# Optimization experiments

Hardware: AMD Instinct MI355X
Metric: run time of the kernel (lower is better)

The kernel has to match this reference:

```python
import jax, jax.numpy as jnp
import numpy as np

NUM_HEADS = 16


def rotate_half(x):
    x1 = x[..., ::2]
    x2 = x[..., 1::2]
    return jnp.concatenate((-x2, x1), axis=-1)


def rope_sin_cos(seq_len, head_dim, dtype):
    inv_freq = 1.0 / (10000.0 ** (jnp.arange(0, head_dim, 2, dtype=jnp.float32) / head_dim))
    t = jnp.arange(seq_len, dtype=jnp.float32)
    freqs = jnp.einsum('i,j->ij', t, inv_freq)          # [S, D/2]
    emb = jnp.concatenate((freqs, freqs), axis=-1)      # [S, D]
    return jnp.sin(emb).astype(dtype), jnp.cos(emb).astype(dtype)


def setup_inputs() -> dict:
    key = jax.random.key(0)
    B, S, E = 2, 2048, 2048
    ks = jax.random.split(key, 5)
    scale = 1.0 / np.sqrt(E)
    return {
        'x': jax.random.normal(ks[0], (B, S, E), dtype=jnp.float32),
        'mask': jnp.ones((B, S), dtype=jnp.int32),
        'Wq': jax.random.normal(ks[1], (E, E), dtype=jnp.float32) * scale,
        'bq': jnp.zeros((E,), dtype=jnp.float32),
        'Wk': jax.random.normal(ks[2], (E, E), dtype=jnp.float32) * scale,
        'bk': jnp.zeros((E,), dtype=jnp.float32),
        'Wv': jax.random.normal(ks[3], (E, E), dtype=jnp.float32) * scale,
        'bv': jnp.zeros((E,), dtype=jnp.float32),
        'Wo': jax.random.normal(ks[4], (E, E), dtype=jnp.float32) * scale,
        'bo': jnp.zeros((E,), dtype=jnp.float32),
    }


def reference(x, mask, Wq, bq, Wk, bk, Wv, bv, Wo, bo):
    B, S, E = x.shape
    H = NUM_HEADS
    D = E // H
    q = (x @ Wq + bq).reshape(B, S, H, D).transpose(0, 2, 1, 3)  # [B,H,S,D]
    k = (x @ Wk + bk).reshape(B, S, H, D).transpose(0, 2, 1, 3)
    v = (x @ Wv + bv).reshape(B, S, H, D).transpose(0, 2, 1, 3)

    sin, cos = rope_sin_cos(S, D, q.dtype)  # [S,D]
    sin = sin[None, None]                    # [1,1,S,D]
    cos = cos[None, None]
    q = q * cos + rotate_half(q) * sin
    k = k * cos + rotate_half(k) * sin

    scores = jnp.einsum('bhqd,bhkd->bhqk', q, k) / jnp.sqrt(jnp.asarray(D, q.dtype))
    scores = jnp.where(mask[:, None, None, :] == 0, -jnp.inf, scores)
    probs = jax.nn.softmax(scores, axis=-1)
    attn = jnp.einsum('bhqk,bhkd->bhqd', probs, v)       # [B,H,S,D]
    attn = attn.transpose(0, 2, 1, 3).reshape(B, S, E)
    return attn @ Wo + bo
```

## Files before the change

### kernel.cpp

```cpp
#include <hip/hip_runtime.h>
#include <hip/hip_bf16.h>
#include <cmath>

typedef unsigned short u16;
typedef unsigned int   u32;

using v4f    = __attribute__((ext_vector_type(4)))  float;
using f32x16 = __attribute__((ext_vector_type(16))) float;
using s8v    = __attribute__((ext_vector_type(8)))  short;
using u32x2  = __attribute__((ext_vector_type(2)))  unsigned int;

union Frag { uint4 u; s8v s; };

__device__ __forceinline__ u16 f2bf(float f){
  u32 u = __float_as_uint(f);
  u32 r = u + 0x7fffu + ((u >> 16) & 1u);
  return (u16)(r >> 16);
}
__device__ __forceinline__ float bf2f(u16 h){ return __uint_as_float(((u32)h) << 16); }

__device__ __forceinline__ u32 cvtpk(float a, float b){
  u32 r;
  asm("v_cvt_pk_bf16_f32 %0, %1, %2" : "=v"(r) : "v"(a), "v"(b));
  return r;
}

__device__ __forceinline__ void async16(const void* g, void* l){
  __builtin_amdgcn_global_load_lds((__attribute__((address_space(1))) void*)g,
                                   (__attribute__((address_space(3))) void*)l, 16, 0, 0);
}

__global__ __launch_bounds__(256) void cast_x_kernel(const float* __restrict__ x, u16* __restrict__ xb){
  size_t i = ((size_t)blockIdx.x * 256 + threadIdx.x) * 4;
  float4 v = *(const float4*)(x + i);
  uint2 o;
  o.x = (u32)f2bf(v.x) | ((u32)f2bf(v.y) << 16);
  o.y = (u32)f2bf(v.z) | ((u32)f2bf(v.w) << 16);
  *(uint2*)(xb + i) = o;
}

__global__ __launch_bounds__(256) void cast_transpose_kernel(
    const float* __restrict__ W0, const float* __restrict__ W1,
    const float* __restrict__ W2, const float* __restrict__ W3,
    u16* __restrict__ T0, u16* __restrict__ T1, u16* __restrict__ T2, u16* __restrict__ T3){
  __shared__ float tile[64][65];
  const float* W = (blockIdx.z==0)?W0:(blockIdx.z==1)?W1:(blockIdx.z==2)?W2:W3;
  u16*         T = (blockIdx.z==0)?T0:(blockIdx.z==1)?T1:(blockIdx.z==2)?T2:T3;
  const int k0 = blockIdx.y*64, n0 = blockIdx.x*64;
  const int t  = threadIdx.x;
  const int rr = t >> 4, c4 = (t & 15) * 4;
  #pragma unroll
  for (int i=0;i<4;i++){
    int k = rr + i*16;
    float4 v = *(const float4*)(W + (size_t)(k0+k)*2048 + n0 + c4);
    tile[k][c4+0]=v.x; tile[k][c4+1]=v.y; tile[k][c4+2]=v.z; tile[k][c4+3]=v.w;
  }
  __syncthreads();
  #pragma unroll
  for (int i=0;i<4;i++){
    int n = rr + i*16;
    uint2 o;
    o.x = (u32)f2bf(tile[c4+0][n]) | ((u32)f2bf(tile[c4+1][n])<<16);
    o.y = (u32)f2bf(tile[c4+2][n]) | ((u32)f2bf(tile[c4+3][n])<<16);
    *(uint2*)(T + (size_t)(n0+n)*2048 + k0 + c4) = o;
  }
}

template<int MODE>
__device__ __forceinline__ void gemm_tile(const u16* __restrict__ A, const u16* __restrict__ BT,
                                          const float* __restrict__ bias, void* __restrict__ Cout,
                                          int m0, int n0, u16* Asl, u16* Bsl){
  constexpr int K = 2048;
  const int tid  = threadIdx.x;
  const int w    = tid >> 6;
  const int lane = tid & 63;
  const int r    = lane & 15, q = lane >> 4;
  const int wm   = (w >> 1) * 64, wn = (w & 1) * 64;

  v4f acc[4][4];
  #pragma unroll
  for (int i=0;i<4;i++)
    #pragma unroll
    for (int j=0;j<4;j++) acc[i][j] = (v4f)0.f;

  const int srow = w*32 + (lane>>3);
  const int sblk = (lane&7) ^ ((lane>>3)&7);
  const u16* Ag = A  + (size_t)(m0+srow)*K + sblk*8;
  const u16* Bg = BT + (size_t)(n0+srow)*K + sblk*8;
  u16* Als = Asl + (w*32)*64;
  u16* Bls = Bsl + (w*32)*64;

  for (int kk = 0; kk < K; kk += 64) {
    #pragma unroll
    for (int i=0;i<4;i++){
      async16(Ag + (size_t)i*8*K + kk, Als + i*512);
      async16(Bg + (size_t)i*8*K + kk, Bls + i*512);
    }
    __syncthreads();
    #pragma unroll
    for (int ks=0; ks<2; ++ks) {
      s8v af[4], bfr[4];
      #pragma unroll
      for (int i=0;i<4;i++){
        int rho = wm + i*16 + r;
        int p = (ks*4 + q) ^ (r&7);
        Frag t; t.u = *(const uint4*)(Asl + rho*64 + p*8); af[i] = t.s;
      }
      #pragma unroll
      for (int j=0;j<4;j++){
        int rho = wn + j*16 + r;
        int p = (ks*4 + q) ^ (r&7);
        Frag t; t.u = *(const uint4*)(Bsl + rho*64 + p*8); bfr[j] = t.s;
      }
      #pragma unroll
      for (int i=0;i<4;i++)
        #pragma unroll
        for (int j=0;j<4;j++)
          acc[i][j] = __builtin_amdgcn_mfma_f32_16x16x32_bf16(af[i], bfr[j], acc[i][j], 0, 0, 0);
    }
    __syncthreads();
  }

  float bv[4];
  #pragma unroll
  for (int j=0;j<4;j++) bv[j] = bias[n0 + wn + j*16 + r];

  #pragma unroll
  for (int i=0;i<4;i++){
    #pragma unroll
    for (int j=0;j<4;j++){
      const int gn = n0 + wn + j*16 + r;
      #pragma unroll
      for (int rr2=0; rr2<4; ++rr2){
        const int gm = m0 + wm + i*16 + q*4 + rr2;
        float val = acc[i][j][rr2] + bv[j];
        if (MODE == 0) ((u16*)Cout)[(size_t)gm*2048 + gn] = f2bf(val);
        else           ((float*)Cout)[(size_t)gm*2048 + gn] = val;
      }
    }
  }
}

__global__ __launch_bounds__(256) void gemm_qkv_kernel(
    const u16* __restrict__ A,
    const u16* __restrict__ WqT, const u16* __restrict__ WkT, const u16* __restrict__ WvT,
    const float* __restrict__ bq, const float* __restrict__ bk, const float* __restrict__ bv,
    u16* __restrict__ Qb, u16* __restrict__ Kb, u16* __restrict__ Vb){
  __shared__ u16 Asl[128*64];
  __shared__ u16 Bsl[128*64];
  const int mat = blockIdx.x >> 4;
  const u16*   BT   = (mat==0)?WqT:(mat==1)?WkT:WvT;
  const float* bias = (mat==0)?bq :(mat==1)?bk :bv;
  u16*         Cout = (mat==0)?Qb :(mat==1)?Kb :Vb;
  gemm_tile<0>(A, BT, bias, Cout, blockIdx.y*128, (blockIdx.x & 15)*128, Asl, Bsl);
}

template<int MODE>
__global__ __launch_bounds__(256) void gemm_kernel(const u16* __restrict__ A,
                                                   const u16* __restrict__ BT,
                                                   const float* __restrict__ bias,
                                                   void* __restrict__ Cout){
  __shared__ u16 Asl[128*64];
  __shared__ u16 Bsl[128*64];
  gemm_tile<MODE>(A, BT, bias, Cout, blockIdx.y*128, blockIdx.x*128, Asl, Bsl);
}

__global__ __launch_bounds__(256) void rope_kernel(u16* __restrict__ Q, u16* __restrict__ Kb){
  const int wrow = blockIdx.x*4 + (threadIdx.x >> 6);
  const int lane = threadIdx.x & 63;
  u16* P = (blockIdx.y == 0) ? Q : Kb;
  const int s = (wrow >> 4) & 2047;
  const size_t base = (size_t)wrow * 128;
  float invf = exp2f(-(float)lane * 0.20762050593045952f);
  float angle = (float)s * invf;
  float sn, cs;
  sincosf(angle, &sn, &cs);
  float x_j   = bf2f(P[base + lane]);
  float x_j64 = bf2f(P[base + 64 + lane]);
  float x_2j  = bf2f(P[base + 2*lane]);
  float x_2j1 = bf2f(P[base + 2*lane + 1]);
  float o0 = x_j  * cs - x_2j1 * sn;
  float o1 = x_j64 * cs + x_2j  * sn;
  P[base + lane]      = f2bf(o0);
  P[base + 64 + lane] = f2bf(o1);
}

__global__ __launch_bounds__(256) void transpose_v_kernel(const u16* __restrict__ V, u16* __restrict__ VT){
  __shared__ u16 t[64*72];
  const int s0 = blockIdx.x*64;
  const int d0 = blockIdx.y*64;
  const int bh = blockIdx.z;
  const int b = bh >> 4, h = bh & 15;
  const size_t obase = ((size_t)bh*128 + d0)*2048 + s0;
  const int tid = threadIdx.x;
  #pragma unroll
  for (int i=0;i<2;i++){
    int c = tid + i*256;
    int sl = c >> 3, dc = (c & 7) * 8;
    *(uint4*)(t + sl*72 + dc) =
      *(const uint4*)(V + ((size_t)(b*2048 + s0 + sl))*2048 + h*128 + d0 + dc);
  }
  __syncthreads();
  #pragma unroll
  for (int i=0;i<2;i++){
    int c = tid + i*256;
    int dl = c >> 3, sc4 = (c & 7) * 8;
    u16 tmp[8];
    #pragma unroll
    for (int j=0;j<8;j++) tmp[j] = t[(sc4+j)*72 + dl];
    *(uint4*)(VT + obase + (size_t)dl*2048 + sc4) = *(const uint4*)tmp;
  }
}

__global__ __launch_bounds__(256,2) void attn_kernel(const u16* __restrict__ Q,
                                                     const u16* __restrict__ K,
                                                     const u16* __restrict__ VT,
                                                     const int* __restrict__ mask,
                                                     u16* __restrict__ Out){
  constexpr int S = 2048;
  constexpr float SL2 = 0.08838834764831845f * 1.4426950408889634f;
  __shared__ u16 smem[32768];

  const int tid = threadIdx.x, w = tid >> 6, lane = tid & 63;
  const int qc = lane & 31;
  const int h  = lane >> 5;
  const int l7 = lane & 7;
  const int hh = blockIdx.y, b = blockIdx.z;
  const int q0 = blockIdx.x * 128;
  const size_t rowb = (size_t)b * 2048;
  const size_t bhD  = ((size_t)(b*16 + hh)) * 128;

  s8v qf[8];
  {
    const u16* qp = Q + (rowb + q0 + w*32 + qc)*2048 + hh*128 + h*8;
    #pragma unroll
    for (int t=0;t<8;t++){ Frag f; f.u = *(const uint4*)(qp + t*16); qf[t] = f.s; }
  }

  f32x16 accO[4];
  #pragma unroll
  for (int d=0; d<4; d++) accO[d] = (f32x16)0.f;
  float lsum = 0.f;

  const int sr4 = lane >> 4, sp16 = lane & 15;
  const int vr8 = lane >> 3, vp8 = lane & 7;

  auto stage = [&](u16* base, int key0){
    u16* Kd = base;
    u16* Vd = base + 8192;
    #pragma unroll
    for (int i=0;i<4;i++){
      int R = w*16 + i*4;
      int ob = sp16 ^ ((R&7) + sr4);
      async16(K + (rowb + key0 + R + sr4)*2048 + hh*128 + ob*8, Kd + R*128);
    }
    #pragma unroll
    for (int i=0;i<4;i++){
      int R = w*32 + i*8;
      int ob = vp8 ^ vr8;
      async16(VT + (bhD + R + vr8)*2048 + key0 + ob*8, Vd + R*64);
    }
  };

  stage(smem, 0);
  int mv = mask[b*S + lane];
  __syncthreads();
  unsigned long long bm = __ballot(mv != 0);
  int cur = 0;

  for (int it=0; it<32; ++it){
    if (it < 31){
      stage(smem + (cur^1)*16384, (it+1)*64);
      mv = mask[b*S + (it+1)*64 + lane];
    }
    const u16* Ks = smem + cur*16384;
    const u16* Vs = Ks + 8192;

    #pragma unroll
    for (int nb=0; nb<2; ++nb){
      f32x16 sc = (f32x16)0.f;
      __builtin_amdgcn_s_setprio(1);
      #pragma unroll
      for (int t=0;t<8;t++){
        Frag kf; kf.u = *(const uint4*)(Ks + (nb*32 + qc)*128 + (((2*t + h) ^ l7)*8));
        sc = __builtin_amdgcn_mfma_f32_32x32x16_bf16(kf.s, qf[t], sc, 0, 0, 0);
      }
      __builtin_amdgcn_s_setprio(0);
      float p[16];
      #pragma unroll
      for (int m=0; m<16; ++m) p[m] = exp2f(sc[m] * SL2);
      if (bm != ~0ull){
        #pragma unroll
        for (int m=0; m<16; ++m){
          int bit = nb*32 + (m&3) + 8*(m>>2) + 4*h;
          if (!((bm >> bit) & 1ull)) p[m] = 0.f;
        }
      }
      #pragma unroll
      for (int m=0; m<16; ++m) lsum += p[m];

      #pragma unroll
      for (int g=0; g<2; ++g){
        u32 a0 = cvtpk(p[8*g+0], p[8*g+1]);
        u32 a1 = cvtpk(p[8*g+2], p[8*g+3]);
        u32 a2 = cvtpk(p[8*g+4], p[8*g+5]);
        u32 a3 = cvtpk(p[8*g+6], p[8*g+7]);
        u32x2 r0 = __builtin_amdgcn_permlane32_swap(a0, a2, false, false);
        u32x2 r1 = __builtin_amdgcn_permlane32_swap(a1, a3, false, false);
        Frag pf; pf.u = make_uint4(r0[0], r1[0], r0[1], r1[1]);
        const int T = nb*2 + g;
        __builtin_amdgcn_s_setprio(1);
        #pragma unroll
        for (int d=0; d<4; ++d){
          Frag vf; vf.u = *(const uint4*)(Vs + (d*32 + qc)*64 + (((2*T + h) ^ l7)*8));
          accO[d] = __builtin_amdgcn_mfma_f32_32x32x16_bf16(vf.s, pf.s, accO[d], 0, 0, 0);
        }
        __builtin_amdgcn_s_setprio(0);
      }
    }
    __syncthreads();
    bm = __ballot(mv != 0);
    cur ^= 1;
  }

  float sall = lsum + __shfl_xor(lsum, 32, 64);
  float invv = (sall > 0.f) ? 1.f/sall : 0.f;
  u16* orow = Out + (rowb + q0 + w*32 + qc)*2048 + hh*128;
  #pragma unroll
  for (int d=0; d<4; ++d){
    #pragma unroll
    for (int g2=0; g2<4; ++g2){
      uint2 o;
      o.x = cvtpk(accO[d][g2*4+0] * invv, accO[d][g2*4+1] * invv);
      o.y = cvtpk(accO[d][g2*4+2] * invv, accO[d][g2*4+3] * invv);
      *(uint2*)(orow + d*32 + g2*8 + 4*h) = o;
    }
  }
}

extern "C" void kernel_launch(void* const* d_in, const int* in_sizes, int n_in,
                              void* d_out, int out_size, void* d_ws, size_t ws_size,
                              hipStream_t stream) {
  (void)in_sizes; (void)n_in; (void)out_size; (void)ws_size;
  const float* x    = (const float*)d_in[0];
  const int*   mask = (const int*)d_in[1];
  const float* Wq   = (const float*)d_in[2];
  const float* bq   = (const float*)d_in[3];
  const float* Wk   = (const float*)d_in[4];
  const float* bk   = (const float*)d_in[5];
  const float* Wv   = (const float*)d_in[6];
  const float* bv   = (const float*)d_in[7];
  const float* Wo   = (const float*)d_in[8];
  const float* bo   = (const float*)d_in[9];

  u16* xbf = (u16*)d_ws;
  u16* WqT = xbf + 8388608;
  u16* WkT = WqT + 4194304;
  u16* WvT = WkT + 4194304;
  u16* WoT = WvT + 4194304;
  u16* Qb  = WoT + 4194304;
  u16* Kb  = Qb + 8388608;
  u16* Vb  = Kb + 8388608;
  u16* Ab  = Vb + 8388608;
  u16* VTb = Ab + 8388608;

  cast_x_kernel<<<8192, 256, 0, stream>>>(x, xbf);
  cast_transpose_kernel<<<dim3(32,32,4), 256, 0, stream>>>(Wq, Wk, Wv, Wo, WqT, WkT, WvT, WoT);
  gemm_qkv_kernel<<<dim3(48,32), 256, 0, stream>>>(xbf, WqT, WkT, WvT, bq, bk, bv, Qb, Kb, Vb);
  rope_kernel<<<dim3(16384,2), 256, 0, stream>>>(Qb, Kb);
  transpose_v_kernel<<<dim3(32,2,32), 256, 0, stream>>>(Vb, VTb);
  attn_kernel<<<dim3(16,16,2), 256, 0, stream>>>(Qb, Kb, VTb, mask, Ab);
  gemm_kernel<1><<<dim3(16,32), 256, 0, stream>>>(Ab, WoT, bo, (float*)d_out);
}
```

Measured before the change: 411.3 us.

## Split attention keys across two wave groups and split-K the output projection

The attention kernel now runs 512 threads per block. Two groups of four waves each process half of every 64-key tile, and their partial sums and accumulators are merged through shared memory at the end. The output projection GEMM is split along K into two halves that write fp32 partials into the freed Q/K workspace, and a new add-bias kernel sums them. This is meant to raise parallelism and occupancy for both kernels, at the cost of a shared-memory reduction, extra partial-buffer traffic and one more launch.

```diff
diff --git a/kernel.cpp b/kernel.cpp
--- a/kernel.cpp
+++ b/kernel.cpp
@@ -69,7 +69,7 @@
 template<int MODE>
 __device__ __forceinline__ void gemm_tile(const u16* __restrict__ A, const u16* __restrict__ BT,
                                           const float* __restrict__ bias, void* __restrict__ Cout,
-                                          int m0, int n0, u16* Asl, u16* Bsl){
+                                          int m0, int n0, int kbeg, int kend, u16* Asl, u16* Bsl){
   constexpr int K = 2048;
   const int tid  = threadIdx.x;
   const int w    = tid >> 6;
@@ -90,7 +90,7 @@
   u16* Als = Asl + (w*32)*64;
   u16* Bls = Bsl + (w*32)*64;
 
-  for (int kk = 0; kk < K; kk += 64) {
+  for (int kk = kbeg; kk < kend; kk += 64) {
     #pragma unroll
     for (int i=0;i<4;i++){
       async16(Ag + (size_t)i*8*K + kk, Als + i*512);
@@ -122,8 +122,13 @@
   }
 
   float bv[4];
-  #pragma unroll
-  for (int j=0;j<4;j++) bv[j] = bias[n0 + wn + j*16 + r];
+  if constexpr (MODE < 2){
+    #pragma unroll
+    for (int j=0;j<4;j++) bv[j] = bias[n0 + wn + j*16 + r];
+  } else {
+    #pragma unroll
+    for (int j=0;j<4;j++) bv[j] = 0.f;
+  }
 
   #pragma unroll
   for (int i=0;i<4;i++){
@@ -152,17 +157,29 @@
   const u16*   BT   = (mat==0)?WqT:(mat==1)?WkT:WvT;
   const float* bias = (mat==0)?bq :(mat==1)?bk :bv;
   u16*         Cout = (mat==0)?Qb :(mat==1)?Kb :Vb;
-  gemm_tile<0>(A, BT, bias, Cout, blockIdx.y*128, (blockIdx.x & 15)*128, Asl, Bsl);
-}
-
-template<int MODE>
-__global__ __launch_bounds__(256) void gemm_kernel(const u16* __restrict__ A,
-                                                   const u16* __restrict__ BT,
-                                                   const float* __restrict__ bias,
-                                                   void* __restrict__ Cout){
+  gemm_tile<0>(A, BT, bias, Cout, blockIdx.y*128, (blockIdx.x & 15)*128, 0, 2048, Asl, Bsl);
+}
+
+__global__ __launch_bounds__(256) void gemm_wo_kernel(const u16* __restrict__ A,
+                                                      const u16* __restrict__ WoT,
+                                                      float* __restrict__ part){
   __shared__ u16 Asl[128*64];
   __shared__ u16 Bsl[128*64];
-  gemm_tile<MODE>(A, BT, bias, Cout, blockIdx.y*128, blockIdx.x*128, Asl, Bsl);
+  const int z = blockIdx.z;
+  gemm_tile<2>(A, WoT, nullptr, part + (size_t)z*8388608,
+               blockIdx.y*128, blockIdx.x*128, z*1024, z*1024+1024, Asl, Bsl);
+}
+
+__global__ __launch_bounds__(256) void add_bias_kernel(const float* __restrict__ p0,
+                                                       const float* __restrict__ p1,
+                                                       const float* __restrict__ bias,
+                                                       float* __restrict__ out){
+  size_t i = ((size_t)blockIdx.x * 256 + threadIdx.x) * 4;
+  float4 a = *(const float4*)(p0 + i);
+  float4 b = *(const float4*)(p1 + i);
+  float4 c = *(const float4*)(bias + (i & 2047));
+  float4 o; o.x = a.x+b.x+c.x; o.y = a.y+b.y+c.y; o.z = a.z+b.z+c.z; o.w = a.w+b.w+c.w;
+  *(float4*)(out + i) = o;
 }
 
 __global__ __launch_bounds__(256) void rope_kernel(u16* __restrict__ Q, u16* __restrict__ Kb){
@@ -212,7 +229,7 @@
   }
 }
 
-__global__ __launch_bounds__(256,2) void attn_kernel(const u16* __restrict__ Q,
+__global__ __launch_bounds__(512,4) void attn_kernel(const u16* __restrict__ Q,
                                                      const u16* __restrict__ K,
                                                      const u16* __restrict__ VT,
                                                      const int* __restrict__ mask,
@@ -222,6 +239,8 @@
   __shared__ u16 smem[32768];
 
   const int tid = threadIdx.x, w = tid >> 6, lane = tid & 63;
+  const int wg  = w & 3;
+  const int grp = w >> 2;
   const int qc = lane & 31;
   const int h  = lane >> 5;
   const int l7 = lane & 7;
@@ -232,7 +251,7 @@
 
   s8v qf[8];
   {
-    const u16* qp = Q + (rowb + q0 + w*32 + qc)*2048 + hh*128 + h*8;
+    const u16* qp = Q + (rowb + q0 + wg*32 + qc)*2048 + hh*128 + h*8;
     #pragma unroll
     for (int t=0;t<8;t++){ Frag f; f.u = *(const uint4*)(qp + t*16); qf[t] = f.s; }
   }
@@ -249,14 +268,14 @@
     u16* Kd = base;
     u16* Vd = base + 8192;
     #pragma unroll
-    for (int i=0;i<4;i++){
-      int R = w*16 + i*4;
+    for (int i=0;i<2;i++){
+      int R = w*8 + i*4;
       int ob = sp16 ^ ((R&7) + sr4);
       async16(K + (rowb + key0 + R + sr4)*2048 + hh*128 + ob*8, Kd + R*128);
     }
     #pragma unroll
-    for (int i=0;i<4;i++){
-      int R = w*32 + i*8;
+    for (int i=0;i<2;i++){
+      int R = w*16 + i*8;
       int ob = vp8 ^ vr8;
       async16(VT + (bhD + R + vr8)*2048 + key0 + ob*8, Vd + R*64);
     }
@@ -276,64 +295,86 @@
     const u16* Ks = smem + cur*16384;
     const u16* Vs = Ks + 8192;
 
-    #pragma unroll
-    for (int nb=0; nb<2; ++nb){
-      f32x16 sc = (f32x16)0.f;
+    f32x16 sc = (f32x16)0.f;
+    __builtin_amdgcn_s_setprio(1);
+    #pragma unroll
+    for (int t=0;t<8;t++){
+      Frag kf; kf.u = *(const uint4*)(Ks + (grp*32 + qc)*128 + (((2*t + h) ^ l7)*8));
+      sc = __builtin_amdgcn_mfma_f32_32x32x16_bf16(kf.s, qf[t], sc, 0, 0, 0);
+    }
+    __builtin_amdgcn_s_setprio(0);
+    float p[16];
+    #pragma unroll
+    for (int m=0; m<16; ++m) p[m] = exp2f(sc[m] * SL2);
+    if (bm != ~0ull){
+      #pragma unroll
+      for (int m=0; m<16; ++m){
+        int bit = grp*32 + (m&3) + 8*(m>>2) + 4*h;
+        if (!((bm >> bit) & 1ull)) p[m] = 0.f;
+      }
+    }
+    #pragma unroll
+    for (int m=0; m<16; ++m) lsum += p[m];
+
+    #pragma unroll
+    for (int gi=0; gi<2; ++gi){
+      u32 a0 = cvtpk(p[8*gi+0], p[8*gi+1]);
+      u32 a1 = cvtpk(p[8*gi+2], p[8*gi+3]);
+      u32 a2 = cvtpk(p[8*gi+4], p[8*gi+5]);
+      u32 a3 = cvtpk(p[8*gi+6], p[8*gi+7]);
+      u32x2 r0 = __builtin_amdgcn_permlane32_swap(a0, a2, false, false);
+      u32x2 r1 = __builtin_amdgcn_permlane32_swap(a1, a3, false, false);
+      Frag pf; pf.u = make_uint4(r0[0], r1[0], r0[1], r1[1]);
+      const int T = grp*2 + gi;
       __builtin_amdgcn_s_setprio(1);
       #pragma unroll
-      for (int t=0;t<8;t++){
-        Frag kf; kf.u = *(const uint4*)(Ks + (nb*32 + qc)*128 + (((2*t + h) ^ l7)*8));
-        sc = __builtin_amdgcn_mfma_f32_32x32x16_bf16(kf.s, qf[t], sc, 0, 0, 0);
+      for (int d=0; d<4; ++d){
+        Frag vf; vf.u = *(const uint4*)(Vs + (d*32 + qc)*64 + (((2*T + h) ^ l7)*8));
+        accO[d] = __builtin_amdgcn_mfma_f32_32x32x16_bf16(vf.s, pf.s, accO[d], 0, 0, 0);
       }
       __builtin_amdgcn_s_setprio(0);
-      float p[16];
-      #pragma unroll
-      for (int m=0; m<16; ++m) p[m] = exp2f(sc[m] * SL2);
-      if (bm != ~0ull){
-        #pragma unroll
-        for (int m=0; m<16; ++m){
-          int bit = nb*32 + (m&3) + 8*(m>>2) + 4*h;
-          if (!((bm >> bit) & 1ull)) p[m] = 0.f;
-        }
-      }
-      #pragma unroll
-      for (int m=0; m<16; ++m) lsum += p[m];
-
-      #pragma unroll
-      for (int g=0; g<2; ++g){
-        u32 a0 = cvtpk(p[8*g+0], p[8*g+1]);
-        u32 a1 = cvtpk(p[8*g+2], p[8*g+3]);
-        u32 a2 = cvtpk(p[8*g+4], p[8*g+5]);
-        u32 a3 = cvtpk(p[8*g+6], p[8*g+7]);
-        u32x2 r0 = __builtin_amdgcn_permlane32_swap(a0, a2, false, false);
-        u32x2 r1 = __builtin_amdgcn_permlane32_swap(a1, a3, false, false);
-        Frag pf; pf.u = make_uint4(r0[0], r1[0], r0[1], r1[1]);
-        const int T = nb*2 + g;
-        __builtin_amdgcn_s_setprio(1);
-        #pragma unroll
-        for (int d=0; d<4; ++d){
-          Frag vf; vf.u = *(const uint4*)(Vs + (d*32 + qc)*64 + (((2*T + h) ^ l7)*8));
-          accO[d] = __builtin_amdgcn_mfma_f32_32x32x16_bf16(vf.s, pf.s, accO[d], 0, 0, 0);
-        }
-        __builtin_amdgcn_s_setprio(0);
-      }
     }
     __syncthreads();
     bm = __ballot(mv != 0);
     cur ^= 1;
   }
 
-  float sall = lsum + __shfl_xor(lsum, 32, 64);
-  float invv = (sall > 0.f) ? 1.f/sall : 0.f;
-  u16* orow = Out + (rowb + q0 + w*32 + qc)*2048 + hh*128;
-  #pragma unroll
-  for (int d=0; d<4; ++d){
-    #pragma unroll
-    for (int g2=0; g2<4; ++g2){
-      uint2 o;
-      o.x = cvtpk(accO[d][g2*4+0] * invv, accO[d][g2*4+1] * invv);
-      o.y = cvtpk(accO[d][g2*4+2] * invv, accO[d][g2*4+3] * invv);
-      *(uint2*)(orow + d*32 + g2*8 + 4*h) = o;
+  float sg = lsum + __shfl_xor(lsum, 32, 64);
+  float* red = (float*)smem;
+  __syncthreads();
+  if (grp == 1) red[wg*64 + lane] = sg;
+  __syncthreads();
+  float invv = 0.f;
+  if (grp == 0){
+    float tot = sg + red[wg*64 + lane];
+    invv = (tot > 0.f) ? 1.f/tot : 0.f;
+  }
+  __syncthreads();
+  if (grp == 1){
+    float* dst = red + wg*4096;
+    #pragma unroll
+    for (int d=0; d<4; ++d)
+      #pragma unroll
+      for (int j=0; j<16; ++j) dst[(d*16+j)*64 + lane] = accO[d][j];
+  }
+  __syncthreads();
+  if (grp == 0){
+    const float* src = red + wg*4096;
+    #pragma unroll
+    for (int d=0; d<4; ++d)
+      #pragma unroll
+      for (int j=0; j<16; ++j) accO[d][j] += src[(d*16+j)*64 + lane];
+
+    u16* orow = Out + (rowb + q0 + wg*32 + qc)*2048 + hh*128;
+    #pragma unroll
+    for (int d=0; d<4; ++d){
+      #pragma unroll
+      for (int g2=0; g2<4; ++g2){
+        uint2 o;
+        o.x = cvtpk(accO[d][g2*4+0] * invv, accO[d][g2*4+1] * invv);
+        o.y = cvtpk(accO[d][g2*4+2] * invv, accO[d][g2*4+3] * invv);
+        *(uint2*)(orow + d*32 + g2*8 + 4*h) = o;
+      }
     }
   }
 }
@@ -361,14 +402,16 @@
   u16* Qb  = WoT + 4194304;
   u16* Kb  = Qb + 8388608;
   u16* Vb  = Kb + 8388608;
-  u16* Ab  = Vb + 8388608;
-  u16* VTb = Ab + 8388608;
+  u16* VTb = Vb + 8388608;
+  u16* Ab  = VTb + 8388608;
+  float* part = (float*)Qb;
 
   cast_x_kernel<<<8192, 256, 0, stream>>>(x, xbf);
   cast_transpose_kernel<<<dim3(32,32,4), 256, 0, stream>>>(Wq, Wk, Wv, Wo, WqT, WkT, WvT, WoT);
   gemm_qkv_kernel<<<dim3(48,32), 256, 0, stream>>>(xbf, WqT, WkT, WvT, bq, bk, bv, Qb, Kb, Vb);
   rope_kernel<<<dim3(16384,2), 256, 0, stream>>>(Qb, Kb);
   transpose_v_kernel<<<dim3(32,2,32), 256, 0, stream>>>(Vb, VTb);
-  attn_kernel<<<dim3(16,16,2), 256, 0, stream>>>(Qb, Kb, VTb, mask, Ab);
-  gemm_kernel<1><<<dim3(16,32), 256, 0, stream>>>(Ab, WoT, bo, (float*)d_out);
-}
+  attn_kernel<<<dim3(16,16,2), 512, 0, stream>>>(Qb, Kb, VTb, mask, Ab);
+  gemm_wo_kernel<<<dim3(16,32,2), 256, 0, stream>>>(Ab, WoT, part);
+  add_bias_kernel<<<8192, 256, 0, stream>>>(part, part + 8388608, bo, (float*)d_out);
+}
```

New measurement: 596.3 us. 45.0% more time.

## Merge prep and rope/transpose kernels into single launches, swizzle GEMM block order

Applied to the files above, without the earlier changes.

Combines the x cast and weight cast-transpose into one launch, and RoPE with the V transpose into another, by splitting a flat 1D grid into ranges. This cuts kernel launches and the gaps between them. It also remaps GEMM block indices so that every 8th linear block shares a tile region, which is meant to improve L2 reuse across CUs/XCDs. Buffer ordering in the workspace changes but sizes stay the same.

```diff
diff --git a/kernel.cpp b/kernel.cpp
--- a/kernel.cpp
+++ b/kernel.cpp
@@ -30,23 +30,27 @@
                                    (__attribute__((address_space(3))) void*)l, 16, 0, 0);
 }
 
-__global__ __launch_bounds__(256) void cast_x_kernel(const float* __restrict__ x, u16* __restrict__ xb){
-  size_t i = ((size_t)blockIdx.x * 256 + threadIdx.x) * 4;
-  float4 v = *(const float4*)(x + i);
-  uint2 o;
-  o.x = (u32)f2bf(v.x) | ((u32)f2bf(v.y) << 16);
-  o.y = (u32)f2bf(v.z) | ((u32)f2bf(v.w) << 16);
-  *(uint2*)(xb + i) = o;
-}
-
-__global__ __launch_bounds__(256) void cast_transpose_kernel(
+__global__ __launch_bounds__(256) void prep_kernel(
+    const float* __restrict__ x, u16* __restrict__ xb,
     const float* __restrict__ W0, const float* __restrict__ W1,
     const float* __restrict__ W2, const float* __restrict__ W3,
     u16* __restrict__ T0, u16* __restrict__ T1, u16* __restrict__ T2, u16* __restrict__ T3){
   __shared__ float tile[64][65];
-  const float* W = (blockIdx.z==0)?W0:(blockIdx.z==1)?W1:(blockIdx.z==2)?W2:W3;
-  u16*         T = (blockIdx.z==0)?T0:(blockIdx.z==1)?T1:(blockIdx.z==2)?T2:T3;
-  const int k0 = blockIdx.y*64, n0 = blockIdx.x*64;
+  const int bid = blockIdx.x;
+  if (bid < 8192){
+    size_t i = ((size_t)bid * 256 + threadIdx.x) * 4;
+    float4 v = *(const float4*)(x + i);
+    uint2 o;
+    o.x = (u32)f2bf(v.x) | ((u32)f2bf(v.y) << 16);
+    o.y = (u32)f2bf(v.z) | ((u32)f2bf(v.w) << 16);
+    *(uint2*)(xb + i) = o;
+    return;
+  }
+  const int t4 = bid - 8192;
+  const int z  = t4 >> 10;
+  const float* W = (z==0)?W0:(z==1)?W1:(z==2)?W2:W3;
+  u16*         T = (z==0)?T0:(z==1)?T1:(z==2)?T2:T3;
+  const int k0 = ((t4 & 1023) >> 5)*64, n0 = (t4 & 31)*64;
   const int t  = threadIdx.x;
   const int rr = t >> 4, c4 = (t & 15) * 4;
   #pragma unroll
@@ -148,48 +152,58 @@
     u16* __restrict__ Qb, u16* __restrict__ Kb, u16* __restrict__ Vb){
   __shared__ u16 Asl[128*64];
   __shared__ u16 Bsl[128*64];
-  const int mat = blockIdx.x >> 4;
+  const int L   = blockIdx.x + 48*blockIdx.y;
+  const int wid = (L & 7)*192 + (L >> 3);
+  const int bx  = wid % 48, by = wid / 48;
+  const int mat = bx >> 4;
   const u16*   BT   = (mat==0)?WqT:(mat==1)?WkT:WvT;
   const float* bias = (mat==0)?bq :(mat==1)?bk :bv;
   u16*         Cout = (mat==0)?Qb :(mat==1)?Kb :Vb;
-  gemm_tile<0>(A, BT, bias, Cout, blockIdx.y*128, (blockIdx.x & 15)*128, Asl, Bsl);
-}
-
-template<int MODE>
-__global__ __launch_bounds__(256) void gemm_kernel(const u16* __restrict__ A,
-                                                   const u16* __restrict__ BT,
-                                                   const float* __restrict__ bias,
-                                                   void* __restrict__ Cout){
+  gemm_tile<0>(A, BT, bias, Cout, by*128, (bx & 15)*128, Asl, Bsl);
+}
+
+__global__ __launch_bounds__(256) void gemm_wo_kernel(const u16* __restrict__ A,
+                                                      const u16* __restrict__ WoT,
+                                                      const float* __restrict__ bias,
+                                                      float* __restrict__ out){
   __shared__ u16 Asl[128*64];
   __shared__ u16 Bsl[128*64];
-  gemm_tile<MODE>(A, BT, bias, Cout, blockIdx.y*128, blockIdx.x*128, Asl, Bsl);
-}
-
-__global__ __launch_bounds__(256) void rope_kernel(u16* __restrict__ Q, u16* __restrict__ Kb){
-  const int wrow = blockIdx.x*4 + (threadIdx.x >> 6);
-  const int lane = threadIdx.x & 63;
-  u16* P = (blockIdx.y == 0) ? Q : Kb;
-  const int s = (wrow >> 4) & 2047;
-  const size_t base = (size_t)wrow * 128;
-  float invf = exp2f(-(float)lane * 0.20762050593045952f);
-  float angle = (float)s * invf;
-  float sn, cs;
-  sincosf(angle, &sn, &cs);
-  float x_j   = bf2f(P[base + lane]);
-  float x_j64 = bf2f(P[base + 64 + lane]);
-  float x_2j  = bf2f(P[base + 2*lane]);
-  float x_2j1 = bf2f(P[base + 2*lane + 1]);
-  float o0 = x_j  * cs - x_2j1 * sn;
-  float o1 = x_j64 * cs + x_2j  * sn;
-  P[base + lane]      = f2bf(o0);
-  P[base + 64 + lane] = f2bf(o1);
-}
-
-__global__ __launch_bounds__(256) void transpose_v_kernel(const u16* __restrict__ V, u16* __restrict__ VT){
+  const int L   = blockIdx.x + 16*blockIdx.y;
+  const int wid = (L & 7)*64 + (L >> 3);
+  const int bx  = wid % 16, by = wid / 16;
+  gemm_tile<1>(A, WoT, bias, out, by*128, bx*128, Asl, Bsl);
+}
+
+__global__ __launch_bounds__(256) void rope_tv_kernel(u16* __restrict__ Q, u16* __restrict__ Kb,
+                                                      const u16* __restrict__ V, u16* __restrict__ VT){
   __shared__ u16 t[64*72];
-  const int s0 = blockIdx.x*64;
-  const int d0 = blockIdx.y*64;
-  const int bh = blockIdx.z;
+  const int bid = blockIdx.x;
+  if (bid < 32768){
+    const int ry = bid >> 14;
+    const int rx = bid & 16383;
+    const int wrow = rx*4 + (threadIdx.x >> 6);
+    const int lane = threadIdx.x & 63;
+    u16* P = (ry == 0) ? Q : Kb;
+    const int s = (wrow >> 4) & 2047;
+    const size_t base = (size_t)wrow * 128;
+    float invf = exp2f(-(float)lane * 0.20762050593045952f);
+    float angle = (float)s * invf;
+    float sn, cs;
+    sincosf(angle, &sn, &cs);
+    float x_j   = bf2f(P[base + lane]);
+    float x_j64 = bf2f(P[base + 64 + lane]);
+    float x_2j  = bf2f(P[base + 2*lane]);
+    float x_2j1 = bf2f(P[base + 2*lane + 1]);
+    float o0 = x_j  * cs - x_2j1 * sn;
+    float o1 = x_j64 * cs + x_2j  * sn;
+    P[base + lane]      = f2bf(o0);
+    P[base + 64 + lane] = f2bf(o1);
+    return;
+  }
+  const int tb = bid - 32768;
+  const int s0 = (tb & 31)*64;
+  const int d0 = ((tb >> 5) & 1)*64;
+  const int bh = tb >> 6;
   const int b = bh >> 4, h = bh & 15;
   const size_t obase = ((size_t)bh*128 + d0)*2048 + s0;
   const int tid = threadIdx.x;
@@ -361,14 +375,12 @@
   u16* Qb  = WoT + 4194304;
   u16* Kb  = Qb + 8388608;
   u16* Vb  = Kb + 8388608;
-  u16* Ab  = Vb + 8388608;
-  u16* VTb = Ab + 8388608;
-
-  cast_x_kernel<<<8192, 256, 0, stream>>>(x, xbf);
-  cast_transpose_kernel<<<dim3(32,32,4), 256, 0, stream>>>(Wq, Wk, Wv, Wo, WqT, WkT, WvT, WoT);
+  u16* VTb = Vb + 8388608;
+  u16* Ab  = VTb + 8388608;
+
+  prep_kernel<<<12288, 256, 0, stream>>>(x, xbf, Wq, Wk, Wv, Wo, WqT, WkT, WvT, WoT);
   gemm_qkv_kernel<<<dim3(48,32), 256, 0, stream>>>(xbf, WqT, WkT, WvT, bq, bk, bv, Qb, Kb, Vb);
-  rope_kernel<<<dim3(16384,2), 256, 0, stream>>>(Qb, Kb);
-  transpose_v_kernel<<<dim3(32,2,32), 256, 0, stream>>>(Vb, VTb);
+  rope_tv_kernel<<<34816, 256, 0, stream>>>(Qb, Kb, Vb, VTb);
   attn_kernel<<<dim3(16,16,2), 256, 0, stream>>>(Qb, Kb, VTb, mask, Ab);
-  gemm_kernel<1><<<dim3(16,32), 256, 0, stream>>>(Ab, WoT, bo, (float*)d_out);
-}
+  gemm_wo_kernel<<<dim3(16,32), 256, 0, stream>>>(Ab, WoT, bo, (float*)d_out);
+}
```

Result: slower. 419.6 us (+2.0%).
